# Performance work log

Hardware: AMD Instinct MI355X
Metric: run time of the kernel (lower is better)

Reference implementation:

```python
import jax, jax.numpy as jnp
import numpy as np

BETA = 0.25


def setup_inputs() -> dict:
    key = jax.random.key(0)
    k1, k2 = jax.random.split(key)
    z = jax.random.normal(k1, (16, 64, 64, 64), dtype=jnp.float32)        # [B, e_dim, H, W]
    codebook = jax.random.normal(k2, (2048, 64), dtype=jnp.float32)       # [n_e, e_dim]
    return {"z": z, "codebook": codebook}


def reference(z, codebook):
    B, C, H, W = z.shape
    n_e = codebook.shape[0]
    sg = jax.lax.stop_gradient

    zp = jnp.transpose(z, (0, 2, 3, 1))                # [B, H, W, C]
    zf = zp.reshape(-1, C)                             # [N, C]

    # nearest-code logits (inner product; CE in source is dead code)
    logits = zf @ codebook.T                           # [N, n_e]
    idx = jnp.argmax(logits, axis=1)                   # [N]

    z_q = codebook[idx].reshape(zp.shape)              # [B, H, W, C]

    # commitment + codebook loss (this overwrites the CE loss in the source)
    loss = BETA * jnp.mean((sg(z_q) - zp) ** 2) + jnp.mean((z_q - sg(zp)) ** 2)

    # straight-through estimator
    z_q_st = zp + sg(z_q - zp)

    # perplexity via one-hot mean (scatter-add instead of dense one-hot)
    counts = jnp.zeros((n_e,), dtype=zp.dtype).at[idx].add(1.0)
    e_mean = counts / idx.shape[0]
    perplexity = jnp.exp(-jnp.sum(e_mean * jnp.log(e_mean + 1e-10)))

    indices = idx.reshape(B, H * W).astype(jnp.int32)
    z_q_out = jnp.transpose(z_q_st, (0, 3, 1, 2))      # back to [B, C, H, W]
    return z_q_out, loss, perplexity, indices
```

## Files before the change

### kernel.cpp

```cpp
#include <hip/hip_runtime.h>

#define C_DIM   64
#define HW      4096
#define NROWS   65536
#define N_E     2048
#define N_ELEM  4194304
#define OUT_LOSS_OFF 4194304
#define OUT_PPL_OFF  4194305
#define OUT_IDX_OFF  4194306

#define ROWS_B   64
#define NBLOCKS  (NROWS / ROWS_B)
#define NTILE_W  64
#define TILE_U   384

typedef __attribute__((ext_vector_type(8))) short bf16x8;
typedef __attribute__((ext_vector_type(4))) float f32x4;

__device__ __forceinline__ unsigned short f2bf(float f) {
    unsigned u = __float_as_uint(f);
    return (unsigned short)((u + 0x7FFFu + ((u >> 16) & 1u)) >> 16);
}
__device__ __forceinline__ float bf2f(unsigned short b) {
    return __uint_as_float(((unsigned)b) << 16);
}

__global__ __launch_bounds__(256) void vq_prep(
    const float* __restrict__ cb, unsigned short* __restrict__ cbp,
    int* __restrict__ counts, float* __restrict__ loss_accum,
    int* __restrict__ done)
{
    const int u = blockIdx.x * 256 + threadIdx.x;
    if (u < N_E) counts[u] = 0;
    if (u == 0)  { *loss_accum = 0.f; *done = 0; }
    const int c = u >> 6, k = u & 63;
    const float v = cb[u];
    const unsigned short s1 = f2bf(v);
    const float r1 = v - bf2f(s1);
    const unsigned short s2 = f2bf(r1);
    const float r2 = r1 - bf2f(s2);
    const unsigned short s3 = f2bf(r2);
    const int tile = c >> 4, k2 = k >> 5, kk = k & 31;
    const int lane = (kk >> 3) * 16 + (c & 15), i = kk & 7;
    const int base = ((tile * 3 + 0) * 2 + k2) * 512 + lane * 8 + i;
    cbp[base]        = s1;
    cbp[base + 1024] = s2;
    cbp[base + 2048] = s3;
}

#define M16(A_, B_, C_) __builtin_amdgcn_mfma_f32_16x16x32_bf16((A_), (B_), (C_), 0, 0, 0)

#define PASS8(AA, ACC, NT)                                                      \
    ACC = M16(AA[0], zf[0][NT][0], ACC); ACC = M16(AA[1], zf[0][NT][1], ACC);   \
    ACC = M16(AA[0], zf[1][NT][0], ACC); ACC = M16(AA[1], zf[1][NT][1], ACC);   \
    ACC = M16(AA[2], zf[0][NT][0], ACC); ACC = M16(AA[3], zf[0][NT][1], ACC);   \
    ACC = M16(AA[2], zf[1][NT][0], ACC); ACC = M16(AA[3], zf[1][NT][1], ACC);   \
    ACC = M16(AA[0], zf[2][NT][0], ACC); ACC = M16(AA[1], zf[2][NT][1], ACC);   \
    ACC = M16(AA[4], zf[0][NT][0], ACC); ACC = M16(AA[5], zf[0][NT][1], ACC);   \
    ACC = M16(AA[2], zf[2][NT][0], ACC); ACC = M16(AA[3], zf[2][NT][1], ACC);   \
    ACC = M16(AA[4], zf[1][NT][0], ACC); ACC = M16(AA[5], zf[1][NT][1], ACC);

#define COMPUTE_TILE(T_, AA)                                                    \
    {                                                                           \
        f32x4 acc0 = zero4, acc1 = zero4;                                       \
        PASS8(AA, acc0, 0)                                                      \
        PASS8(AA, acc1, 1)                                                      \
        const int cbase = ch * 1024 + (T_) * 16 + lg * 4;                       \
        _Pragma("unroll")                                                       \
        for (int r = 0; r < 4; ++r) {                                           \
            if (acc0[r] > best0) { best0 = acc0[r]; bi0 = cbase + r; }          \
            if (acc1[r] > best1) { best1 = acc1[r]; bi1 = cbase + r; }          \
        }                                                                       \
    }

__global__ __launch_bounds__(256, 4) void vq_mfma(
    const float* __restrict__ z, const float* __restrict__ cb,
    const unsigned short* __restrict__ cbp, float* __restrict__ out,
    int* __restrict__ counts, float* __restrict__ loss_accum,
    int* __restrict__ done)
{
    __shared__ float sbest[2][ROWS_B];
    __shared__ int   sbi[2][ROWS_B];
    __shared__ int   sidx[ROWS_B];
    __shared__ float wsum[4];
    __shared__ int   slast;

    const int tid  = threadIdx.x;
    const int lane = tid & 63;
    const int wv   = tid >> 6;
    const int l15  = lane & 15, lg = lane >> 4;
    const int rh   = wv >> 1;
    const int ch   = wv & 1;
    const int row0 = blockIdx.x * ROWS_B;
    const int b    = row0 >> 12;
    const int hw0  = row0 & 4095;
    const float* zb = z + (size_t)b * C_DIM * HW + hw0;

    if (tid == 0) slast = 0;

    bf16x8 zf[3][2][2];
#pragma unroll
    for (int nt = 0; nt < 2; ++nt) {
        const int row_l = rh * 32 + nt * 16 + l15;
#pragma unroll
        for (int k2 = 0; k2 < 2; ++k2) {
#pragma unroll
            for (int i = 0; i < 8; ++i) {
                float v = zb[(size_t)(k2 * 32 + lg * 8 + i) * HW + row_l];
                unsigned short s1 = f2bf(v);
                float r1 = v - bf2f(s1);
                unsigned short s2 = f2bf(r1);
                float r2 = r1 - bf2f(s2);
                zf[0][nt][k2][i] = (short)s1;
                zf[1][nt][k2][i] = (short)s2;
                zf[2][nt][k2][i] = (short)f2bf(r2);
            }
        }
    }

    const bf16x8* cbpf = (const bf16x8*)cbp + (size_t)ch * NTILE_W * TILE_U;
    float best0 = -3.4e38f, best1 = -3.4e38f;
    int   bi0 = 0, bi1 = 0;
    const f32x4 zero4 = {0.f, 0.f, 0.f, 0.f};

    bf16x8 Acur[6], Anxt[6];
#pragma unroll
    for (int f = 0; f < 6; ++f) Acur[f] = cbpf[f * 64 + lane];

#pragma unroll 1
    for (int t = 0; t < NTILE_W; t += 2) {
#pragma unroll
        for (int f = 0; f < 6; ++f)
            Anxt[f] = cbpf[(size_t)(t + 1) * TILE_U + f * 64 + lane];

        COMPUTE_TILE(t, Acur)

        if (t + 2 < NTILE_W) {
#pragma unroll
            for (int f = 0; f < 6; ++f)
                Acur[f] = cbpf[(size_t)(t + 2) * TILE_U + f * 64 + lane];
        }

        COMPUTE_TILE(t + 1, Anxt)
    }

#pragma unroll
    for (int off = 16; off <= 32; off <<= 1) {
        float ob; int oi;
        ob = __shfl_xor(best0, off, 64); oi = __shfl_xor(bi0, off, 64);
        if (ob > best0 || (ob == best0 && oi < bi0)) { best0 = ob; bi0 = oi; }
        ob = __shfl_xor(best1, off, 64); oi = __shfl_xor(bi1, off, 64);
        if (ob > best1 || (ob == best1 && oi < bi1)) { best1 = ob; bi1 = oi; }
    }
    if (lane < 32) {
        const int nt = lane >> 4;
        const int row_l = rh * 32 + lane;
        sbest[ch][row_l] = (nt == 0) ? best0 : best1;
        sbi[ch][row_l]   = (nt == 0) ? bi0   : bi1;
    }
    __syncthreads();
    if (tid < ROWS_B) {
        float b0 = sbest[0][tid], b1 = sbest[1][tid];
        int   i0 = sbi[0][tid],   i1 = sbi[1][tid];
        const int ii = (b1 > b0) ? i1 : i0;
        sidx[tid] = ii;
        out[OUT_IDX_OFF + row0 + tid] = (float)ii;
        atomicAdd(&counts[ii], 1);
    }
    __syncthreads();

    float* ob0 = out + (size_t)b * C_DIM * HW + hw0;
    float lsum = 0.f;
#pragma unroll
    for (int j = 0; j < 4; ++j) {
        const int m = j * 256 + tid;
        const int r = m & 63, c4 = m >> 6;
        const float4 q4 = *(const float4*)(cb + (size_t)sidx[r] * C_DIM + c4 * 4);
#pragma unroll
        for (int q = 0; q < 4; ++q) {
            const int c = c4 * 4 + q;
            const float zv = zb[(size_t)c * HW + r];
            const float qv = (q == 0) ? q4.x : (q == 1) ? q4.y : (q == 2) ? q4.z : q4.w;
            const float d = qv - zv;
            lsum += d * d;
            ob0[(size_t)c * HW + r] = zv + d;
        }
    }
    for (int off = 32; off > 0; off >>= 1) lsum += __shfl_down(lsum, off, 64);
    if (lane == 0) wsum[wv] = lsum;
    __syncthreads();

    if (tid == 0) {
        atomicAdd(loss_accum, wsum[0] + wsum[1] + wsum[2] + wsum[3]);
        __threadfence();
        const int tk = atomicAdd(done, 1);
        if (tk == NBLOCKS - 1) slast = 1;
    }
    __syncthreads();
    if (slast) {
        __threadfence();
        float h = 0.f;
        for (int e = tid; e < N_E; e += 256) {
            const int cnt = atomicAdd(&counts[e], 0);
            const float em = (float)cnt * (1.0f / (float)NROWS);
            h -= em * logf(em + 1e-10f);
        }
        for (int off = 32; off > 0; off >>= 1) h += __shfl_down(h, off, 64);
        if (lane == 0) wsum[wv] = h;
        __syncthreads();
        if (tid == 0) {
            const float H = wsum[0] + wsum[1] + wsum[2] + wsum[3];
            const float L = atomicAdd(loss_accum, 0.f);
            const float m = L * (1.0f / (float)N_ELEM);
            out[OUT_LOSS_OFF] = 0.25f * m + m;
            out[OUT_PPL_OFF]  = expf(H);
        }
    }
}

extern "C" void kernel_launch(void* const* d_in, const int* in_sizes, int n_in,
                              void* d_out, int out_size, void* d_ws, size_t ws_size,
                              hipStream_t stream)
{
    const float* z  = (const float*)d_in[0];
    const float* cb = (const float*)d_in[1];
    float* out = (float*)d_out;

    int*            counts     = (int*)d_ws;
    float*          loss_accum = (float*)((char*)d_ws + N_E * sizeof(int));
    int*            done       = (int*)((char*)d_ws + N_E * sizeof(int) + 4);
    unsigned short* cbp        = (unsigned short*)((char*)d_ws + 16384);

    vq_prep<<<N_E * C_DIM / 256, 256, 0, stream>>>(cb, cbp, counts, loss_accum, done);
    vq_mfma<<<NBLOCKS, 256, 0, stream>>>(z, cb, cbp, out, counts, loss_accum, done);
}
```

Baseline: 188.6 us.

## Give each wave full codebook per row strip, deepen prefetch, vectorize prep

Each block now handles 128 rows, and each wave scans the whole codebook for its own 32 rows. Previously two waves split the codebook in half, which needed a shared-memory merge and an extra barrier. The main loop now keeps three tiles of codebook fragments in flight with a 4-deep register ring to hide load latency. The prep kernel packs fragments with vector loads and stores in 64 blocks. Trade-offs: occupancy bound drops to 2 blocks per SM with higher register use, each wave's scan loop is twice as long, and only half as many blocks are launched.

```diff
diff --git a/kernel.cpp b/kernel.cpp
--- a/kernel.cpp
+++ b/kernel.cpp
@@ -9,9 +9,9 @@
 #define OUT_PPL_OFF  4194305
 #define OUT_IDX_OFF  4194306
 
-#define ROWS_B   64
+#define ROWS_B   128
 #define NBLOCKS  (NROWS / ROWS_B)
-#define NTILE_W  64
+#define NTILE    (N_E / 16)
 #define TILE_U   384
 
 typedef __attribute__((ext_vector_type(8))) short bf16x8;
@@ -33,19 +33,32 @@
     const int u = blockIdx.x * 256 + threadIdx.x;
     if (u < N_E) counts[u] = 0;
     if (u == 0)  { *loss_accum = 0.f; *done = 0; }
-    const int c = u >> 6, k = u & 63;
-    const float v = cb[u];
-    const unsigned short s1 = f2bf(v);
-    const float r1 = v - bf2f(s1);
-    const unsigned short s2 = f2bf(r1);
-    const float r2 = r1 - bf2f(s2);
-    const unsigned short s3 = f2bf(r2);
-    const int tile = c >> 4, k2 = k >> 5, kk = k & 31;
-    const int lane = (kk >> 3) * 16 + (c & 15), i = kk & 7;
-    const int base = ((tile * 3 + 0) * 2 + k2) * 512 + lane * 8 + i;
-    cbp[base]        = s1;
-    cbp[base + 1024] = s2;
-    cbp[base + 2048] = s3;
+
+    const int lane = u & 63;
+    const int k2   = (u >> 6) & 1;
+    const int tile = u >> 7;
+    const int c    = tile * 16 + (lane & 15);
+    const int k0   = k2 * 32 + (lane >> 4) * 8;
+
+    const float4 va = *(const float4*)(cb + (size_t)c * C_DIM + k0);
+    const float4 vb = *(const float4*)(cb + (size_t)c * C_DIM + k0 + 4);
+    const float v[8] = {va.x, va.y, va.z, va.w, vb.x, vb.y, vb.z, vb.w};
+
+    bf16x8 s1v, s2v, s3v;
+#pragma unroll
+    for (int i = 0; i < 8; ++i) {
+        const unsigned short s1 = f2bf(v[i]);
+        const float r1 = v[i] - bf2f(s1);
+        const unsigned short s2 = f2bf(r1);
+        const float r2 = r1 - bf2f(s2);
+        s1v[i] = (short)s1;
+        s2v[i] = (short)s2;
+        s3v[i] = (short)f2bf(r2);
+    }
+    const size_t base = ((size_t)(tile * 3 + 0) * 2 + k2) * 512 + (size_t)lane * 8;
+    *(bf16x8*)(cbp + base)        = s1v;
+    *(bf16x8*)(cbp + base + 1024) = s2v;
+    *(bf16x8*)(cbp + base + 2048) = s3v;
 }
 
 #define M16(A_, B_, C_) __builtin_amdgcn_mfma_f32_16x16x32_bf16((A_), (B_), (C_), 0, 0, 0)
@@ -65,7 +78,7 @@
         f32x4 acc0 = zero4, acc1 = zero4;                                       \
         PASS8(AA, acc0, 0)                                                      \
         PASS8(AA, acc1, 1)                                                      \
-        const int cbase = ch * 1024 + (T_) * 16 + lg * 4;                       \
+        const int cbase = (T_) * 16 + lg * 4;                                   \
         _Pragma("unroll")                                                       \
         for (int r = 0; r < 4; ++r) {                                           \
             if (acc0[r] > best0) { best0 = acc0[r]; bi0 = cbase + r; }          \
@@ -73,14 +86,19 @@
         }                                                                       \
     }
 
-__global__ __launch_bounds__(256, 4) void vq_mfma(
+#define LOADA(AA, T_)                                                           \
+    {                                                                           \
+        const bf16x8* p_ = cbpf + (size_t)(T_) * TILE_U;                        \
+        _Pragma("unroll")                                                       \
+        for (int f = 0; f < 6; ++f) AA[f] = p_[f * 64 + lane];                  \
+    }
+
+__global__ __launch_bounds__(256, 2) void vq_mfma(
     const float* __restrict__ z, const float* __restrict__ cb,
     const unsigned short* __restrict__ cbp, float* __restrict__ out,
     int* __restrict__ counts, float* __restrict__ loss_accum,
     int* __restrict__ done)
 {
-    __shared__ float sbest[2][ROWS_B];
-    __shared__ int   sbi[2][ROWS_B];
     __shared__ int   sidx[ROWS_B];
     __shared__ float wsum[4];
     __shared__ int   slast;
@@ -89,8 +107,6 @@
     const int lane = tid & 63;
     const int wv   = tid >> 6;
     const int l15  = lane & 15, lg = lane >> 4;
-    const int rh   = wv >> 1;
-    const int ch   = wv & 1;
     const int row0 = blockIdx.x * ROWS_B;
     const int b    = row0 >> 12;
     const int hw0  = row0 & 4095;
@@ -101,7 +117,7 @@
     bf16x8 zf[3][2][2];
 #pragma unroll
     for (int nt = 0; nt < 2; ++nt) {
-        const int row_l = rh * 32 + nt * 16 + l15;
+        const int row_l = wv * 32 + nt * 16 + l15;
 #pragma unroll
         for (int k2 = 0; k2 < 2; ++k2) {
 #pragma unroll
@@ -118,30 +134,24 @@
         }
     }
 
-    const bf16x8* cbpf = (const bf16x8*)cbp + (size_t)ch * NTILE_W * TILE_U;
+    const bf16x8* cbpf = (const bf16x8*)cbp;
     float best0 = -3.4e38f, best1 = -3.4e38f;
     int   bi0 = 0, bi1 = 0;
     const f32x4 zero4 = {0.f, 0.f, 0.f, 0.f};
 
-    bf16x8 Acur[6], Anxt[6];
-#pragma unroll
-    for (int f = 0; f < 6; ++f) Acur[f] = cbpf[f * 64 + lane];
+    bf16x8 A0[6], A1[6], A2[6], A3[6];
+    LOADA(A0, 0) LOADA(A1, 1) LOADA(A2, 2)
 
 #pragma unroll 1
-    for (int t = 0; t < NTILE_W; t += 2) {
-#pragma unroll
-        for (int f = 0; f < 6; ++f)
-            Anxt[f] = cbpf[(size_t)(t + 1) * TILE_U + f * 64 + lane];
-
-        COMPUTE_TILE(t, Acur)
-
-        if (t + 2 < NTILE_W) {
-#pragma unroll
-            for (int f = 0; f < 6; ++f)
-                Acur[f] = cbpf[(size_t)(t + 2) * TILE_U + f * 64 + lane];
-        }
-
-        COMPUTE_TILE(t + 1, Anxt)
+    for (int t = 0; t < NTILE; t += 4) {
+        const int p3 = t + 3;
+        const int p4 = (t + 4 < NTILE) ? t + 4 : NTILE - 1;
+        const int p5 = (t + 5 < NTILE) ? t + 5 : NTILE - 1;
+        const int p6 = (t + 6 < NTILE) ? t + 6 : NTILE - 1;
+        LOADA(A3, p3) COMPUTE_TILE(t,     A0)
+        LOADA(A0, p4) COMPUTE_TILE(t + 1, A1)
+        LOADA(A1, p5) COMPUTE_TILE(t + 2, A2)
+        LOADA(A2, p6) COMPUTE_TILE(t + 3, A3)
     }
 
 #pragma unroll
@@ -154,17 +164,10 @@
     }
     if (lane < 32) {
         const int nt = lane >> 4;
-        const int row_l = rh * 32 + lane;
-        sbest[ch][row_l] = (nt == 0) ? best0 : best1;
-        sbi[ch][row_l]   = (nt == 0) ? bi0   : bi1;
-    }
-    __syncthreads();
-    if (tid < ROWS_B) {
-        float b0 = sbest[0][tid], b1 = sbest[1][tid];
-        int   i0 = sbi[0][tid],   i1 = sbi[1][tid];
-        const int ii = (b1 > b0) ? i1 : i0;
-        sidx[tid] = ii;
-        out[OUT_IDX_OFF + row0 + tid] = (float)ii;
+        const int row_l = wv * 32 + lane;
+        const int ii = (nt == 0) ? bi0 : bi1;
+        sidx[row_l] = ii;
+        out[OUT_IDX_OFF + row0 + row_l] = (float)ii;
         atomicAdd(&counts[ii], 1);
     }
     __syncthreads();
@@ -172,9 +175,9 @@
     float* ob0 = out + (size_t)b * C_DIM * HW + hw0;
     float lsum = 0.f;
 #pragma unroll
-    for (int j = 0; j < 4; ++j) {
+    for (int j = 0; j < 8; ++j) {
         const int m = j * 256 + tid;
-        const int r = m & 63, c4 = m >> 6;
+        const int r = m & 127, c4 = m >> 7;
         const float4 q4 = *(const float4*)(cb + (size_t)sidx[r] * C_DIM + c4 * 4);
 #pragma unroll
         for (int q = 0; q < 4; ++q) {
@@ -231,6 +234,6 @@
     int*            done       = (int*)((char*)d_ws + N_E * sizeof(int) + 4);
     unsigned short* cbp        = (unsigned short*)((char*)d_ws + 16384);
 
-    vq_prep<<<N_E * C_DIM / 256, 256, 0, stream>>>(cb, cbp, counts, loss_accum, done);
+    vq_prep<<<64, 256, 0, stream>>>(cb, cbp, counts, loss_accum, done);
     vq_mfma<<<NBLOCKS, 256, 0, stream>>>(z, cb, cbp, out, counts, loss_accum, done);
 }
```

New measurement: 188.1 us. About the same (-0.3%).
